# Kernel tuning notes

Measured on AMD Instinct MI355X. Metric: run time of the kernel, lower is better.

The kernel has to match this reference:

```python
import jax, jax.numpy as jnp
import numpy as np

B, S, H, HKV, D = 2, 1024, 32, 8, 128


def _rope_tables(seq_len, head_dim, base=10000.0):
    inv_freq = 1.0 / (base ** (np.arange(0, head_dim, 2, dtype=np.float32) / head_dim))
    freqs = np.arange(seq_len, dtype=np.float32)[:, None] * inv_freq[None, :]  # [S, D/2]
    emb = np.concatenate([freqs, freqs], axis=-1)  # [S, D] (Llama layout)
    return jnp.asarray(np.cos(emb)), jnp.asarray(np.sin(emb))


def setup_inputs() -> dict:
    key = jax.random.key(0)
    kq, kk, kv = jax.random.split(key, 3)
    q = jax.random.normal(kq, (B, S, H, D), dtype=jnp.float32)
    k = jax.random.normal(kk, (B, S, HKV, D), dtype=jnp.float32)
    v = jax.random.normal(kv, (B, S, HKV, D), dtype=jnp.float32)
    cos, sin = _rope_tables(S, D)
    # additive causal mask [B, 1, S, S]: 0 where allowed, large negative where masked
    causal = jnp.tril(jnp.ones((S, S), dtype=bool))
    mask = jnp.where(causal, 0.0, -1e9).astype(jnp.float32)
    attention_mask = jnp.broadcast_to(mask[None, None], (B, 1, S, S))
    softmax_scale = 1.0 / float(np.sqrt(D))
    return {
        "query_states": q, "key_states": k, "value_states": v,
        "cos": cos, "sin": sin, "attention_mask": attention_mask,
        "softmax_scale": softmax_scale,
    }


def _apply_rope(x, cos, sin):
    # x: [B, S, h, D]; cos/sin: [S, D]
    d2 = x.shape[-1] // 2
    rot = jnp.concatenate([-x[..., d2:], x[..., :d2]], axis=-1)  # rotate_half
    return x * cos[None, :, None, :] + rot * sin[None, :, None, :]


def reference(query_states, key_states, value_states, cos, sin, attention_mask, softmax_scale):
    b, s, h, d = query_states.shape
    hkv = key_states.shape[2]
    g = h // hkv  # GQA group size
    q = _apply_rope(query_states, cos, sin)
    k = _apply_rope(key_states, cos, sin)
    qg = q.reshape(b, s, hkv, g, d)
    # scores: [B, Hkv, G, Q, K]
    scores = jnp.einsum('bqhgd,bkhd->bhgqk', qg, k) * softmax_scale
    scores = scores + attention_mask[:, :, None]  # [B,1,Q,K] -> broadcast over (Hkv, G)
    p = jax.nn.softmax(scores, axis=-1)
    out = jnp.einsum('bhgqk,bkhd->bqhgd', p, value_states)
    return out.reshape(b, s, h, d)
```

## Files before the change

### kernel.cpp

```cpp
#include <hip/hip_runtime.h>

#define S_LEN 1024
#define D_DIM 128
#define NH    32
#define NKV   8
#define NB    2

typedef __bf16 bf16x8 __attribute__((ext_vector_type(8)));
typedef float  f32x4  __attribute__((ext_vector_type(4)));
typedef unsigned short u16x8 __attribute__((ext_vector_type(8)));

__device__ __forceinline__ unsigned short f2bf(float f) {
    unsigned int u = __float_as_uint(f);
    u += 0x7fffu + ((u >> 16) & 1u);
    return (unsigned short)(u >> 16);
}

__global__ __launch_bounds__(256) void rope_q_kernel(
    const float* __restrict__ q, const float* __restrict__ cosb,
    const float* __restrict__ sinb, const float* __restrict__ scale_ptr,
    unsigned short* __restrict__ Qr)
{
    const float sc = *scale_ptr;
    int gid = blockIdx.x * 256 + threadIdx.x;
    int row = gid >> 6;
    int j   = gid & 63;
    int h  = row & (NH - 1);
    int bs = row >> 5;
    int s  = bs & (S_LEN - 1);
    int b  = bs >> 10;
    const float* qp = q + (size_t)row * D_DIM;
    float x0 = qp[j];
    float x1 = qp[j + 64];
    float c  = cosb[s * D_DIM + j];
    float sn = sinb[s * D_DIM + j];
    size_t orow = ((size_t)(b * NH + h) * S_LEN + s) * D_DIM;
    Qr[orow + j]      = f2bf((x0 * c - x1 * sn) * sc);
    Qr[orow + j + 64] = f2bf((x1 * c + x0 * sn) * sc);
}

__global__ __launch_bounds__(256) void rope_k_kernel(
    const float* __restrict__ k, const float* __restrict__ cosb,
    const float* __restrict__ sinb, unsigned short* __restrict__ Kr)
{
    int gid = blockIdx.x * 256 + threadIdx.x;
    int row = gid >> 6;
    int j   = gid & 63;
    int hk = row & (NKV - 1);
    int bs = row >> 3;
    int s  = bs & (S_LEN - 1);
    int b  = bs >> 10;
    const float* kp = k + (size_t)row * D_DIM;
    float x0 = kp[j];
    float x1 = kp[j + 64];
    float c  = cosb[s * D_DIM + j];
    float sn = sinb[s * D_DIM + j];
    size_t orow = ((size_t)(b * NKV + hk) * S_LEN + s) * D_DIM;
    Kr[orow + j]      = f2bf(x0 * c - x1 * sn);
    Kr[orow + j + 64] = f2bf(x1 * c + x0 * sn);
}

__global__ __launch_bounds__(256) void transpose_v_kernel(
    const float* __restrict__ v, unsigned short* __restrict__ Vt)
{
    int blk   = blockIdx.x;
    int stile = blk & 15;
    int hk    = (blk >> 4) & (NKV - 1);
    int b     = blk >> 7;
    int tid   = threadIdx.x;
    __shared__ unsigned short tile[64][132];
#pragma unroll
    for (int i = 0; i < 8; i++) {
        int e    = i * 256 + tid;
        int srow = e >> 5;
        int dq   = (e & 31) * 4;
        const float* vp = v + (((size_t)(b * S_LEN + stile * 64 + srow) * NKV + hk) * D_DIM + dq);
        float4 val = *(const float4*)vp;
        tile[srow][dq + 0] = f2bf(val.x);
        tile[srow][dq + 1] = f2bf(val.y);
        tile[srow][dq + 2] = f2bf(val.z);
        tile[srow][dq + 3] = f2bf(val.w);
    }
    __syncthreads();
    size_t head = (size_t)(b * NKV + hk) * D_DIM * S_LEN;
#pragma unroll
    for (int i = 0; i < 4; i++) {
        int g  = i * 256 + tid;
        int d  = g >> 3;
        int c8 = g & 7;
        int s0 = c8 * 8;
        u16x8 pk;
#pragma unroll
        for (int jj = 0; jj < 8; jj++) pk[jj] = tile[s0 + jj][d];
        *(u16x8*)(Vt + head + (size_t)d * S_LEN + stile * 64 + s0) = pk;
    }
}

__global__ __launch_bounds__(256) void attn_kernel(
    const unsigned short* __restrict__ Qr,
    const unsigned short* __restrict__ Kr,
    const unsigned short* __restrict__ Vt,
    float* __restrict__ out)
{
    const int p    = blockIdx.x;
    const int h    = blockIdx.y;
    const int b    = blockIdx.z;
    const int hk   = h >> 2;
    const int tid  = threadIdx.x;
    const int w    = tid >> 6;
    const int lane = tid & 63;
    const int lr   = lane & 15;
    const int lg   = lane >> 4;

    __shared__ unsigned short Kt[64 * 128];
    __shared__ unsigned short Vs[128 * 64];
    __shared__ unsigned short Pb[4][16 * 72];

    const unsigned short* khead = Kr + (size_t)(b * NKV + hk) * S_LEN * D_DIM;
    const unsigned short* vhead = Vt + (size_t)(b * NKV + hk) * D_DIM * S_LEN;

    const int krow0 = tid >> 4;
    const int kcc   = tid & 15;
    const int kcs   = kcc ^ (krow0 & 7);
    const int vd0   = tid >> 3;
    const int vcc   = tid & 7;
    const int vcs   = vcc ^ (vd0 & 7);

    u16x8 kreg[4], vreg[4];

    auto issue = [&](int u) {
        const unsigned short* kt = khead + (size_t)u * 64 * D_DIM;
        const unsigned short* vt = vhead + u * 64;
#pragma unroll
        for (int i = 0; i < 4; i++)
            kreg[i] = *(const u16x8*)(kt + (size_t)(krow0 + 16 * i) * D_DIM + kcc * 8);
#pragma unroll
        for (int i = 0; i < 4; i++)
            vreg[i] = *(const u16x8*)(vt + (size_t)(vd0 + 32 * i) * S_LEN + vcc * 8);
    };
    auto commit = [&]() {
#pragma unroll
        for (int i = 0; i < 4; i++)
            *(u16x8*)(&Kt[(krow0 + 16 * i) * 128 + kcs * 8]) = kreg[i];
#pragma unroll
        for (int i = 0; i < 4; i++)
            *(u16x8*)(&Vs[(vd0 + 32 * i) * 64 + vcs * 8]) = vreg[i];
    };

#pragma unroll 1
    for (int pass = 0; pass < 2; ++pass) {
        const int qt = (pass == 0) ? (15 - p) : p;

        const unsigned short* qbase =
            Qr + ((size_t)(b * NH + h) * S_LEN + qt * 64 + w * 16 + lr) * D_DIM;
        bf16x8 qf[4];
#pragma unroll
        for (int kk = 0; kk < 4; kk++)
            qf[kk] = *(const bf16x8*)(qbase + lg * 8 + kk * 32);

        f32x4 o[8];
#pragma unroll
        for (int dt = 0; dt < 8; dt++) o[dt] = f32x4{0.f, 0.f, 0.f, 0.f};
        float m[4], lsum[4];
#pragma unroll
        for (int r = 0; r < 4; r++) { m[r] = -1e30f; lsum[r] = 0.f; }

        issue(0);

#pragma unroll 1
        for (int u = 0; u <= qt; ++u) {
            __syncthreads();
            commit();
            __syncthreads();
            if (u < qt) issue(u + 1);

            f32x4 st[4];
#pragma unroll
            for (int kj = 0; kj < 4; kj++) st[kj] = f32x4{0.f, 0.f, 0.f, 0.f};
#pragma unroll
            for (int kj = 0; kj < 4; kj++) {
                if (u < qt || kj <= w) {
                    int row = kj * 16 + lr;
#pragma unroll
                    for (int kk = 0; kk < 4; kk++) {
                        int cc = lg + kk * 4;
                        int cs = cc ^ (row & 7);
                        bf16x8 kf = *(const bf16x8*)(&Kt[row * 128 + cs * 8]);
                        st[kj] = __builtin_amdgcn_mfma_f32_16x16x32_bf16(qf[kk], kf, st[kj], 0, 0, 0);
                    }
                }
            }
            if (u == qt) {
                int qrow = w * 16 + lg * 4;
#pragma unroll
                for (int kj = 0; kj < 4; kj++) {
                    int col = kj * 16 + lr;
#pragma unroll
                    for (int r = 0; r < 4; r++)
                        if (col > qrow + r) st[kj][r] = -1e30f;
                }
            }

            float pm[4];
#pragma unroll
            for (int r = 0; r < 4; r++) {
                float mx = fmaxf(fmaxf(st[0][r], st[1][r]), fmaxf(st[2][r], st[3][r]));
                mx = fmaxf(mx, __shfl_xor(mx, 1));
                mx = fmaxf(mx, __shfl_xor(mx, 2));
                mx = fmaxf(mx, __shfl_xor(mx, 4));
                mx = fmaxf(mx, __shfl_xor(mx, 8));
                pm[r] = mx;
            }
            bool grew = false;
#pragma unroll
            for (int r = 0; r < 4; r++) grew = grew || (pm[r] > m[r] + 8.f);
            if (__any(grew)) {
#pragma unroll
                for (int r = 0; r < 4; r++) {
                    float mnew = fmaxf(m[r], pm[r]);
                    float ps   = __expf(m[r] - mnew);
                    m[r] = mnew;
                    lsum[r] *= ps;
#pragma unroll
                    for (int dt = 0; dt < 8; dt++) o[dt][r] *= ps;
                }
            }
            float rsum[4] = {0.f, 0.f, 0.f, 0.f};
#pragma unroll
            for (int kj = 0; kj < 4; kj++)
#pragma unroll
                for (int r = 0; r < 4; r++) {
                    float pv = __expf(st[kj][r] - m[r]);
                    st[kj][r] = pv;
                    rsum[r] += pv;
                }
#pragma unroll
            for (int r = 0; r < 4; r++) {
                float s4 = rsum[r];
                s4 += __shfl_xor(s4, 1);
                s4 += __shfl_xor(s4, 2);
                s4 += __shfl_xor(s4, 4);
                s4 += __shfl_xor(s4, 8);
                lsum[r] += s4;
            }

            unsigned short* pbw = &Pb[w][0];
#pragma unroll
            for (int kj = 0; kj < 4; kj++)
#pragma unroll
                for (int r = 0; r < 4; r++)
                    pbw[(lg * 4 + r) * 72 + kj * 16 + lr] = f2bf(st[kj][r]);

#pragma unroll
            for (int kk2 = 0; kk2 < 2; kk2++) {
                bf16x8 pf = *(const bf16x8*)(&pbw[lr * 72 + lg * 8 + kk2 * 32]);
#pragma unroll
                for (int dt = 0; dt < 8; dt++) {
                    int vrow = dt * 16 + lr;
                    int cc = lg + kk2 * 4;
                    int cs = cc ^ (vrow & 7);
                    bf16x8 vf = *(const bf16x8*)(&Vs[vrow * 64 + cs * 8]);
                    o[dt] = __builtin_amdgcn_mfma_f32_16x16x32_bf16(pf, vf, o[dt], 0, 0, 0);
                }
            }
        }

        float inv[4];
#pragma unroll
        for (int r = 0; r < 4; r++) inv[r] = 1.0f / lsum[r];
        float* obase = out + ((size_t)(b * S_LEN + qt * 64 + w * 16) * NH + h) * D_DIM;
#pragma unroll
        for (int dt = 0; dt < 8; dt++)
#pragma unroll
            for (int r = 0; r < 4; r++)
                obase[(size_t)(lg * 4 + r) * NH * D_DIM + dt * 16 + lr] = o[dt][r] * inv[r];
    }
}

extern "C" void kernel_launch(void* const* d_in, const int* in_sizes, int n_in,
                              void* d_out, int out_size, void* d_ws, size_t ws_size,
                              hipStream_t stream) {
    const float* q    = (const float*)d_in[0];
    const float* k    = (const float*)d_in[1];
    const float* v    = (const float*)d_in[2];
    const float* cosb = (const float*)d_in[3];
    const float* sinb = (const float*)d_in[4];
    const float* scale = (const float*)d_in[6];
    float* out = (float*)d_out;

    unsigned short* Qr = (unsigned short*)d_ws;
    unsigned short* Kr = Qr + (size_t)NB * NH  * S_LEN * D_DIM;
    unsigned short* Vt = Kr + (size_t)NB * NKV * S_LEN * D_DIM;

    rope_q_kernel<<<NB * S_LEN * NH / 4, 256, 0, stream>>>(q, cosb, sinb, scale, Qr);
    rope_k_kernel<<<NB * S_LEN * NKV / 4, 256, 0, stream>>>(k, cosb, sinb, Kr);
    transpose_v_kernel<<<NB * NKV * (S_LEN / 64), 256, 0, stream>>>(v, Vt);
    dim3 grid(8, NH, NB);
    attn_kernel<<<grid, 256, 0, stream>>>(Qr, Kr, Vt, out);
}
```

Measured before the change: 74.51 us.

## Double-buffer K/V via direct global-to-LDS loads and transpose QK MFMA layout

Replaces the register-staged K/V prefetch (load to registers, sync, write LDS, sync) with direct global_load_lds into double-buffered shared tiles, removing one barrier per step and the register staging. It also swaps the QK MFMA operands so each lane owns a query column, which cuts the row-max and row-sum shuffles to two each and gives one running max per lane. Scale is folded with log2(e) so exp2f replaces __expf, the P buffer gets a swizzled unpadded layout, and s_setprio wraps the MFMA sections. The doubled LDS use may limit occupancy, and __launch_bounds__(256,2) asks for two blocks per CU. The new scheme depends on correct vmcnt waiting before each barrier.

```diff
diff --git a/kernel.cpp b/kernel.cpp
--- a/kernel.cpp
+++ b/kernel.cpp
@@ -16,12 +16,18 @@
     return (unsigned short)(u >> 16);
 }
 
+__device__ __forceinline__ void gld_lds16(const unsigned short* g, unsigned short* l) {
+    __builtin_amdgcn_global_load_lds(
+        (const __attribute__((address_space(1))) unsigned int*)(g),
+        (__attribute__((address_space(3))) unsigned int*)(l), 16, 0, 0);
+}
+
 __global__ __launch_bounds__(256) void rope_q_kernel(
     const float* __restrict__ q, const float* __restrict__ cosb,
     const float* __restrict__ sinb, const float* __restrict__ scale_ptr,
     unsigned short* __restrict__ Qr)
 {
-    const float sc = *scale_ptr;
+    const float sc = *scale_ptr * 1.44269504088896f;
     int gid = blockIdx.x * 256 + threadIdx.x;
     int row = gid >> 6;
     int j   = gid & 63;
@@ -96,7 +102,7 @@
     }
 }
 
-__global__ __launch_bounds__(256) void attn_kernel(
+__global__ __launch_bounds__(256, 2) void attn_kernel(
     const unsigned short* __restrict__ Qr,
     const unsigned short* __restrict__ Kr,
     const unsigned short* __restrict__ Vt,
@@ -112,39 +118,30 @@
     const int lr   = lane & 15;
     const int lg   = lane >> 4;
 
-    __shared__ unsigned short Kt[64 * 128];
-    __shared__ unsigned short Vs[128 * 64];
-    __shared__ unsigned short Pb[4][16 * 72];
+    __shared__ unsigned short Kt[2][64 * 128];
+    __shared__ unsigned short Vs[2][128 * 64];
+    __shared__ unsigned short Pb[4][16 * 64];
 
     const unsigned short* khead = Kr + (size_t)(b * NKV + hk) * S_LEN * D_DIM;
     const unsigned short* vhead = Vt + (size_t)(b * NKV + hk) * D_DIM * S_LEN;
 
-    const int krow0 = tid >> 4;
-    const int kcc   = tid & 15;
-    const int kcs   = kcc ^ (krow0 & 7);
-    const int vd0   = tid >> 3;
-    const int vcc   = tid & 7;
-    const int vcs   = vcc ^ (vd0 & 7);
-
-    u16x8 kreg[4], vreg[4];
-
-    auto issue = [&](int u) {
+    auto stage = [&](int u, int buf) {
         const unsigned short* kt = khead + (size_t)u * 64 * D_DIM;
+#pragma unroll
+        for (int n = 0; n < 4; n++) {
+            int row = w * 16 + n * 4 + (lane >> 4);
+            int cc  = (lane & 15) ^ (row & 7);
+            gld_lds16(kt + (size_t)row * D_DIM + cc * 8,
+                      &Kt[buf][(w * 16 + n * 4) * 128]);
+        }
         const unsigned short* vt = vhead + u * 64;
 #pragma unroll
-        for (int i = 0; i < 4; i++)
-            kreg[i] = *(const u16x8*)(kt + (size_t)(krow0 + 16 * i) * D_DIM + kcc * 8);
-#pragma unroll
-        for (int i = 0; i < 4; i++)
-            vreg[i] = *(const u16x8*)(vt + (size_t)(vd0 + 32 * i) * S_LEN + vcc * 8);
-    };
-    auto commit = [&]() {
-#pragma unroll
-        for (int i = 0; i < 4; i++)
-            *(u16x8*)(&Kt[(krow0 + 16 * i) * 128 + kcs * 8]) = kreg[i];
-#pragma unroll
-        for (int i = 0; i < 4; i++)
-            *(u16x8*)(&Vs[(vd0 + 32 * i) * 64 + vcs * 8]) = vreg[i];
+        for (int n = 0; n < 4; n++) {
+            int d  = w * 32 + n * 8 + (lane >> 3);
+            int cc = (lane & 7) ^ (d & 7);
+            gld_lds16(vt + (size_t)d * S_LEN + cc * 8,
+                      &Vs[buf][(w * 32 + n * 8) * 64]);
+        }
     };
 
 #pragma unroll 1
@@ -161,119 +158,111 @@
         f32x4 o[8];
 #pragma unroll
         for (int dt = 0; dt < 8; dt++) o[dt] = f32x4{0.f, 0.f, 0.f, 0.f};
-        float m[4], lsum[4];
-#pragma unroll
-        for (int r = 0; r < 4; r++) { m[r] = -1e30f; lsum[r] = 0.f; }
-
-        issue(0);
+        float m_run = -1e30f, lsum = 0.f;
+
+        if (pass) __syncthreads();
+        stage(0, 0);
 
 #pragma unroll 1
         for (int u = 0; u <= qt; ++u) {
+            const int cur = u & 1;
             __syncthreads();
-            commit();
-            __syncthreads();
-            if (u < qt) issue(u + 1);
+            if (u < qt) stage(u + 1, cur ^ 1);
 
             f32x4 st[4];
 #pragma unroll
             for (int kj = 0; kj < 4; kj++) st[kj] = f32x4{0.f, 0.f, 0.f, 0.f};
+            __builtin_amdgcn_s_setprio(1);
 #pragma unroll
             for (int kj = 0; kj < 4; kj++) {
                 if (u < qt || kj <= w) {
                     int row = kj * 16 + lr;
 #pragma unroll
                     for (int kk = 0; kk < 4; kk++) {
-                        int cc = lg + kk * 4;
-                        int cs = cc ^ (row & 7);
-                        bf16x8 kf = *(const bf16x8*)(&Kt[row * 128 + cs * 8]);
-                        st[kj] = __builtin_amdgcn_mfma_f32_16x16x32_bf16(qf[kk], kf, st[kj], 0, 0, 0);
+                        int cs = (lg + kk * 4) ^ (row & 7);
+                        bf16x8 kf = *(const bf16x8*)(&Kt[cur][row * 128 + cs * 8]);
+                        st[kj] = __builtin_amdgcn_mfma_f32_16x16x32_bf16(kf, qf[kk], st[kj], 0, 0, 0);
                     }
                 }
             }
+            __builtin_amdgcn_s_setprio(0);
+
             if (u == qt) {
-                int qrow = w * 16 + lg * 4;
-#pragma unroll
-                for (int kj = 0; kj < 4; kj++) {
-                    int col = kj * 16 + lr;
+#pragma unroll
+                for (int kj = 0; kj < 4; kj++)
 #pragma unroll
                     for (int r = 0; r < 4; r++)
-                        if (col > qrow + r) st[kj][r] = -1e30f;
-                }
-            }
-
-            float pm[4];
-#pragma unroll
-            for (int r = 0; r < 4; r++) {
-                float mx = fmaxf(fmaxf(st[0][r], st[1][r]), fmaxf(st[2][r], st[3][r]));
-                mx = fmaxf(mx, __shfl_xor(mx, 1));
-                mx = fmaxf(mx, __shfl_xor(mx, 2));
-                mx = fmaxf(mx, __shfl_xor(mx, 4));
-                mx = fmaxf(mx, __shfl_xor(mx, 8));
-                pm[r] = mx;
-            }
-            bool grew = false;
-#pragma unroll
-            for (int r = 0; r < 4; r++) grew = grew || (pm[r] > m[r] + 8.f);
-            if (__any(grew)) {
+                        if (kj * 16 + lg * 4 + r > w * 16 + lr) st[kj][r] = -1e30f;
+            }
+
+            float lmax = fmaxf(fmaxf(fmaxf(st[0][0], st[0][1]), fmaxf(st[0][2], st[0][3])),
+                               fmaxf(fmaxf(st[1][0], st[1][1]), fmaxf(st[1][2], st[1][3])));
+            lmax = fmaxf(lmax,
+                   fmaxf(fmaxf(fmaxf(st[2][0], st[2][1]), fmaxf(st[2][2], st[2][3])),
+                         fmaxf(fmaxf(st[3][0], st[3][1]), fmaxf(st[3][2], st[3][3]))));
+            float pm = fmaxf(lmax, __shfl_xor(lmax, 16));
+            pm = fmaxf(pm, __shfl_xor(pm, 32));
+
+            if (__any(pm > m_run + 8.f)) {
+                float mnew = fmaxf(m_run, pm);
+                float ps   = exp2f(m_run - mnew);
+                m_run = mnew;
+                lsum *= ps;
 #pragma unroll
                 for (int r = 0; r < 4; r++) {
-                    float mnew = fmaxf(m[r], pm[r]);
-                    float ps   = __expf(m[r] - mnew);
-                    m[r] = mnew;
-                    lsum[r] *= ps;
-#pragma unroll
-                    for (int dt = 0; dt < 8; dt++) o[dt][r] *= ps;
-                }
-            }
-            float rsum[4] = {0.f, 0.f, 0.f, 0.f};
+                    float psr = __shfl(ps, lg * 4 + r);
+#pragma unroll
+                    for (int dt = 0; dt < 8; dt++) o[dt][r] *= psr;
+                }
+            }
+            float lsloc = 0.f;
 #pragma unroll
             for (int kj = 0; kj < 4; kj++)
 #pragma unroll
                 for (int r = 0; r < 4; r++) {
-                    float pv = __expf(st[kj][r] - m[r]);
+                    float pv = exp2f(st[kj][r] - m_run);
                     st[kj][r] = pv;
-                    rsum[r] += pv;
-                }
-#pragma unroll
-            for (int r = 0; r < 4; r++) {
-                float s4 = rsum[r];
-                s4 += __shfl_xor(s4, 1);
-                s4 += __shfl_xor(s4, 2);
-                s4 += __shfl_xor(s4, 4);
-                s4 += __shfl_xor(s4, 8);
-                lsum[r] += s4;
-            }
-
-            unsigned short* pbw = &Pb[w][0];
-#pragma unroll
-            for (int kj = 0; kj < 4; kj++)
-#pragma unroll
-                for (int r = 0; r < 4; r++)
-                    pbw[(lg * 4 + r) * 72 + kj * 16 + lr] = f2bf(st[kj][r]);
-
+                    lsloc += pv;
+                }
+            float t = lsloc + __shfl_xor(lsloc, 16);
+            t += __shfl_xor(t, 32);
+            lsum += t;
+
+            char* pw = (char*)&Pb[w][0];
+#pragma unroll
+            for (int kj = 0; kj < 4; kj++) {
+                unsigned int w0 = (unsigned)f2bf(st[kj][0]) | ((unsigned)f2bf(st[kj][1]) << 16);
+                unsigned int w1 = (unsigned)f2bf(st[kj][2]) | ((unsigned)f2bf(st[kj][3]) << 16);
+                int C = (2 * kj + (lg >> 1)) ^ (lr & 7);
+                *(uint2*)(pw + lr * 128 + C * 16 + (lg & 1) * 8) = uint2{w0, w1};
+            }
+
+            __builtin_amdgcn_s_setprio(1);
 #pragma unroll
             for (int kk2 = 0; kk2 < 2; kk2++) {
-                bf16x8 pf = *(const bf16x8*)(&pbw[lr * 72 + lg * 8 + kk2 * 32]);
+                int Cp = (lg + 4 * kk2) ^ (lr & 7);
+                bf16x8 pf = *(const bf16x8*)(pw + lr * 128 + Cp * 16);
 #pragma unroll
                 for (int dt = 0; dt < 8; dt++) {
                     int vrow = dt * 16 + lr;
-                    int cc = lg + kk2 * 4;
-                    int cs = cc ^ (vrow & 7);
-                    bf16x8 vf = *(const bf16x8*)(&Vs[vrow * 64 + cs * 8]);
+                    int cs = (lg + kk2 * 4) ^ (vrow & 7);
+                    bf16x8 vf = *(const bf16x8*)(&Vs[cur][vrow * 64 + cs * 8]);
                     o[dt] = __builtin_amdgcn_mfma_f32_16x16x32_bf16(pf, vf, o[dt], 0, 0, 0);
                 }
             }
+            __builtin_amdgcn_s_setprio(0);
         }
 
-        float inv[4];
-#pragma unroll
-        for (int r = 0; r < 4; r++) inv[r] = 1.0f / lsum[r];
+        float rcp = 1.0f / lsum;
+        float invr[4];
+#pragma unroll
+        for (int r = 0; r < 4; r++) invr[r] = __shfl(rcp, lg * 4 + r);
         float* obase = out + ((size_t)(b * S_LEN + qt * 64 + w * 16) * NH + h) * D_DIM;
 #pragma unroll
         for (int dt = 0; dt < 8; dt++)
 #pragma unroll
             for (int r = 0; r < 4; r++)
-                obase[(size_t)(lg * 4 + r) * NH * D_DIM + dt * 16 + lr] = o[dt][r] * inv[r];
+                obase[(size_t)(lg * 4 + r) * NH * D_DIM + dt * 16 + lr] = o[dt][r] * invr[r];
     }
 }
 
```

New measurement: 66.26 us. 11.1% less time.
